# Kernel optimization log

Hardware: AMD Instinct MI355X
Metric: run time of the kernel (lower is better)

The kernel has to match this reference:

```python
import jax, jax.numpy as jnp
import numpy as np

B, S, IN, D, H, K, NLVL = 8, 1536, 32, 128, 4, 7, 2
DFF = 4 * D
DK = D // H
EPS = 1e-6


def setup_inputs() -> dict:
    key = jax.random.key(0)
    ks = jax.random.split(key, 24)
    rn = lambda k, sh, s=0.05: jax.random.normal(k, sh, jnp.float32) * s
    z = lambda sh: jnp.zeros(sh, jnp.float32)
    o = lambda sh: jnp.ones(sh, jnp.float32)
    return {
        'x': jax.random.normal(ks[0], (B, S, IN), jnp.float32),
        'enc_W': rn(ks[1], (IN, D)), 'enc_b': z((D,)),
        'ln_rnn_a': o((NLVL, D)), 'ln_rnn_b': z((NLVL, D)),
        'gru_Wih': rn(ks[2], (NLVL, 3 * D, D)), 'gru_Whh': rn(ks[3], (NLVL, 3 * D, D)),
        'gru_bih': z((NLVL, 3 * D)), 'gru_bhh': z((NLVL, 3 * D)),
        'ln_attn_a': o((NLVL, D)), 'ln_attn_b': z((NLVL, D)),
        'Wq': rn(ks[4], (NLVL, D, D)), 'bq': z((NLVL, D)),
        'Wk': rn(ks[5], (NLVL, D, D)), 'bk': z((NLVL, D)),
        'Wv': rn(ks[6], (NLVL, D, D)), 'bv': z((NLVL, D)),
        'Wo': rn(ks[7], (NLVL, D, D)), 'bo': z((NLVL, D)),
        'ln_ff_a': o((NLVL, D)), 'ln_ff_b': z((NLVL, D)),
        'ff_W1': rn(ks[8], (NLVL, D, DFF)), 'ff_b1': z((NLVL, DFF)),
        'ff_W2': rn(ks[9], (NLVL, DFF, D)), 'ff_b2': z((NLVL, D)),
        'out_W': rn(ks[10], (D, 1)), 'out_b': z((1,)),
    }


def layernorm(x, a, b):
    # faithful to torch code: unbiased std (ddof=1), divide by (std + eps)
    m = x.mean(-1, keepdims=True)
    s = jnp.std(x, axis=-1, ddof=1, keepdims=True)
    return a * (x - m) / (s + EPS) + b


def local_rnn(x, Wih, Whh, bih, bhh):
    # x: [B,S,D]. Window each position into its ksize-length causal window,
    # run a GRU over the window (scan over K steps, batched over B*S), keep last h.
    xp = jnp.pad(x, ((0, 0), (K - 1, 0), (0, 0)))            # zero left-pad
    win = jnp.stack([xp[:, i:i + S] for i in range(K)], 0)   # [K,B,S,D]

    def step(h, xt):
        gi = xt @ Wih.T + bih                                 # [B,S,3D]
        gh = h @ Whh.T + bhh
        ir, iz, inn = jnp.split(gi, 3, -1)
        hr, hz, hn = jnp.split(gh, 3, -1)
        r = jax.nn.sigmoid(ir + hr)
        zz = jax.nn.sigmoid(iz + hz)
        nn_ = jnp.tanh(inn + r * hn)
        return (1.0 - zz) * nn_ + zz * h, None

    h, _ = jax.lax.scan(step, jnp.zeros_like(x), win)
    return h


def mhpool(x, Wq, bq, Wk, bk, Wv, bv, Wo, bo):
    def heads(w, bb):
        return jnp.swapaxes((x @ w + bb).reshape(B, S, H, DK), 1, 2)  # [B,H,S,DK]
    q, k, v = heads(Wq, bq), heads(Wk, bk), heads(Wv, bv)
    scores = jnp.einsum('bhqd,bhkd->bhqk', q, k) / np.float32(np.sqrt(DK))
    mask = jnp.tril(jnp.ones((S, S), bool))
    scores = jnp.where(mask, scores, jnp.float32(-1e9))
    p = jax.nn.softmax(scores, axis=-1)
    o = jnp.einsum('bhqk,bhkd->bhqd', p, v)
    o = jnp.swapaxes(o, 1, 2).reshape(B, S, D)
    return o @ Wo + bo


def reference(x, enc_W, enc_b, ln_rnn_a, ln_rnn_b, gru_Wih, gru_Whh, gru_bih,
              gru_bhh, ln_attn_a, ln_attn_b, Wq, bq, Wk, bk, Wv, bv, Wo, bo,
              ln_ff_a, ln_ff_b, ff_W1, ff_b1, ff_W2, ff_b2, out_W, out_b):
    h = x @ enc_W + enc_b
    for i in range(NLVL):
        # LocalRNNLayer (pre-norm residual); LocalRNN.output Linear is unused in orig forward
        h = h + local_rnn(layernorm(h, ln_rnn_a[i], ln_rnn_b[i]),
                          gru_Wih[i], gru_Whh[i], gru_bih[i], gru_bhh[i])
        # MHPooling sublayer
        h = h + mhpool(layernorm(h, ln_attn_a[i], ln_attn_b[i]),
                       Wq[i], bq[i], Wk[i], bk[i], Wv[i], bv[i], Wo[i], bo[i])
        # PositionwiseFeedForward sublayer
        hn = layernorm(h, ln_ff_a[i], ln_ff_b[i])
        h = h + (jax.nn.relu(hn @ ff_W1[i] + ff_b1[i]) @ ff_W2[i] + ff_b2[i])
    return jax.nn.sigmoid(h @ out_W + out_b)
```

## Files before the change

### kernel.cpp

```cpp
#include <hip/hip_runtime.h>
#include <math.h>

#define DEV_INLINE __device__ __forceinline__

constexpr int B = 8, S = 1536, IN = 32, D = 128, NH = 4, KWIN = 7, NLVL = 2;
constexpr int DFF = 512, DKH = 32;
constexpr int M = B * S;
constexpr int MD = M * D;
constexpr float EPS = 1e-6f;

typedef unsigned short u16;
typedef __bf16 bf16x8 __attribute__((ext_vector_type(8)));
typedef float f32x4 __attribute__((ext_vector_type(4)));
typedef unsigned short u16x4 __attribute__((ext_vector_type(4)));

#define MFMA16(a, b, c) __builtin_amdgcn_mfma_f32_16x16x32_bf16(a, b, c, 0, 0, 0)

DEV_INLINE float sigmoidf_(float x) { return 1.f / (1.f + __expf(-x)); }

DEV_INLINE u16 f2bf(float f) {
    unsigned u = __builtin_bit_cast(unsigned, f);
    unsigned rnd = 0x7FFFu + ((u >> 16) & 1u);
    return (u16)((u + rnd) >> 16);
}
DEV_INLINE float b2f(u16 v) { return __builtin_bit_cast(float, (unsigned)v << 16); }

template <int KDIM>
DEV_INLINE void mfma_tile32(const u16* a0p, const u16* a1p, const u16* b0p, const u16* b1p,
                            f32x4& acc00, f32x4& acc01, f32x4& acc10, f32x4& acc11) {
    #pragma unroll
    for (int k0 = 0; k0 < KDIM; k0 += 32) {
        bf16x8 a0 = *(const bf16x8*)(a0p + k0);
        bf16x8 a1 = *(const bf16x8*)(a1p + k0);
        bf16x8 b0 = *(const bf16x8*)(b0p + k0);
        bf16x8 b1 = *(const bf16x8*)(b1p + k0);
        acc00 = MFMA16(a0, b0, acc00);
        acc01 = MFMA16(a0, b1, acc01);
        acc10 = MFMA16(a1, b0, acc10);
        acc11 = MFMA16(a1, b1, acc11);
    }
}

__global__ __launch_bounds__(256) void k_prep_enc(
    const float* __restrict__ Wih, const float* __restrict__ Whh,
    const float* __restrict__ Wq, const float* __restrict__ Wk,
    const float* __restrict__ Wv, const float* __restrict__ Wo,
    const float* __restrict__ W1, const float* __restrict__ W2,
    u16* __restrict__ Wih16, u16* __restrict__ Whh16,
    u16* __restrict__ Wqkv, u16* __restrict__ WoT,
    u16* __restrict__ W1T, u16* __restrict__ W2T,
    const float* __restrict__ x, const float* __restrict__ encW, const float* __restrict__ encb,
    const float* __restrict__ ga, const float* __restrict__ gb,
    float* __restrict__ h, u16* __restrict__ xnout) {
    __shared__ float xs[32][33];
    __shared__ float Ws[32][128];
    const int tid = threadIdx.x;
    if (blockIdx.x < 2304) {
        constexpr int SZ_GRU = NLVL * 384 * 128;
        constexpr int SZ_DD  = NLVL * 128 * 128;
        constexpr int SZ_FF  = NLVL * 128 * 512;
        int i = blockIdx.x * 256 + tid;
        if (i < SZ_GRU) { Wih16[i] = f2bf(Wih[i]); return; }
        i -= SZ_GRU;
        if (i < SZ_GRU) { Whh16[i] = f2bf(Whh[i]); return; }
        i -= SZ_GRU;
        if (i < 3 * SZ_DD) {
            int seg = i / SZ_DD, j = i - seg * SZ_DD;
            int lvl = j >> 14, rem = j & 16383, k = rem >> 7, n = rem & 127;
            const float* src = seg == 0 ? Wq : (seg == 1 ? Wk : Wv);
            Wqkv[(size_t)lvl * 384 * 128 + (size_t)(seg * 128 + n) * 128 + k] = f2bf(src[j]);
            return;
        }
        i -= 3 * SZ_DD;
        if (i < SZ_DD) {
            int lvl = i >> 14, rem = i & 16383, k = rem >> 7, n = rem & 127;
            WoT[(size_t)lvl * 16384 + n * 128 + k] = f2bf(Wo[i]); return;
        }
        i -= SZ_DD;
        if (i < SZ_FF) {
            int lvl = i >> 16, rem = i & 65535, k = rem >> 9, n = rem & 511;
            W1T[(size_t)lvl * 65536 + n * 128 + k] = f2bf(W1[i]); return;
        }
        i -= SZ_FF;
        if (i < SZ_FF) {
            int lvl = i >> 16, rem = i & 65535, k = rem >> 7, n = rem & 127;
            W2T[(size_t)lvl * 65536 + n * 512 + k] = f2bf(W2[i]); return;
        }
        return;
    }
    const int row0 = (blockIdx.x - 2304) * 32;
    for (int i = tid; i < 32 * 32; i += 256) xs[i >> 5][i & 31] = x[(size_t)row0 * IN + i];
    for (int i = tid; i < 32 * 128; i += 256) Ws[i >> 7][i & 127] = encW[i];
    __syncthreads();
    const int r = tid >> 3, cg = (tid & 7) * 16;
    float acc[16];
    #pragma unroll
    for (int j = 0; j < 16; ++j) acc[j] = encb[cg + j];
    for (int k = 0; k < IN; ++k) {
        const float xv = xs[r][k];
        #pragma unroll
        for (int j = 0; j < 16; ++j) acc[j] = fmaf(xv, Ws[k][cg + j], acc[j]);
    }
    float s = 0.f;
    #pragma unroll
    for (int j = 0; j < 16; ++j) s += acc[j];
    s += __shfl_xor(s, 1); s += __shfl_xor(s, 2); s += __shfl_xor(s, 4);
    const float mean = s * (1.f / D);
    float q = 0.f;
    #pragma unroll
    for (int j = 0; j < 16; ++j) { float d = acc[j] - mean; q += d * d; }
    q += __shfl_xor(q, 1); q += __shfl_xor(q, 2); q += __shfl_xor(q, 4);
    const float inv = 1.f / (sqrtf(q * (1.f / (D - 1))) + EPS);
    float* hp = h + (size_t)(row0 + r) * D + cg;
    u16* xp = xnout + (size_t)(row0 + r) * D + cg;
    #pragma unroll
    for (int jj = 0; jj < 4; ++jj) {
        float4 hv = make_float4(acc[4 * jj], acc[4 * jj + 1], acc[4 * jj + 2], acc[4 * jj + 3]);
        *(float4*)(hp + 4 * jj) = hv;
        u16x4 o;
        #pragma unroll
        for (int c = 0; c < 4; ++c)
            o[c] = f2bf(ga[cg + 4 * jj + c] * (acc[4 * jj + c] - mean) * inv + gb[cg + 4 * jj + c]);
        *(u16x4*)(xp + 4 * jj) = o;
    }
}

__global__ __launch_bounds__(512, 2) void k_gru_qkv(
    const u16* __restrict__ xn,
    const u16* __restrict__ Wih16,
    const u16* __restrict__ Whh16,
    const float* __restrict__ bih, const float* __restrict__ bhh,
    float* __restrict__ hout,
    const float* __restrict__ ga, const float* __restrict__ gb,
    const u16* __restrict__ Wqkv,
    const float* __restrict__ bq, const float* __restrict__ bk, const float* __restrict__ bv,
    u16* __restrict__ q16, u16* __restrict__ k16, u16* __restrict__ vt16) {
    constexpr int RB = 48;
    constexpr float QS = 0.17677669529663687f * 1.4426950408889634f;
    __shared__ __align__(16) u16 xnS[64 * 136];
    __shared__ __align__(16) u16 Gs[64 * 392];
    __shared__ __align__(16) u16 hs16[RB * 136];
    const int tid = threadIdx.x;
    const int wave = tid >> 6, lane = tid & 63;
    const int col16 = lane & 15, quad = lane >> 4;
    const int row0 = blockIdx.x * RB;
    const int ss0 = row0 % S;
    const int cc = wave * 16 + col16;

    for (int i = tid; i < 64 * 16; i += 512) {
        const int r = i >> 4, c8 = (i & 15) * 8;
        bf16x8 val = {};
        if (ss0 - 16 + r >= 0)
            val = *(const bf16x8*)(xn + (size_t)(row0 - 16 + r) * 128 + c8);
        *(bf16x8*)&xnS[r * 136 + c8] = val;
    }
    bf16x8 Breg[3][4];
    #pragma unroll
    for (int g = 0; g < 3; ++g)
        #pragma unroll
        for (int kc = 0; kc < 4; ++kc)
            Breg[g][kc] = *(const bf16x8*)(Whh16 + (size_t)(g * 128 + cc) * 128 + kc * 32 + quad * 8);
    float bi[3], bh[3];
    #pragma unroll
    for (int g = 0; g < 3; ++g) { bi[g] = bih[g * 128 + cc]; bh[g] = bhh[g * 128 + cc]; }
    __syncthreads();

    #pragma unroll
    for (int tt = wave; tt < 24; tt += 8) {
        const int rt = tt / 12, ct = tt - rt * 12;
        const u16* bp = Wih16 + (size_t)(ct * 32 + col16) * 128 + quad * 8;
        f32x4 a00 = {0.f, 0.f, 0.f, 0.f}, a01 = a00, a10 = a00, a11 = a00;
        #pragma unroll
        for (int k0 = 0; k0 < 128; k0 += 32) {
            bf16x8 af0 = *(const bf16x8*)&xnS[(rt * 32 + col16) * 136 + k0 + quad * 8];
            bf16x8 af1 = *(const bf16x8*)&xnS[(rt * 32 + 16 + col16) * 136 + k0 + quad * 8];
            bf16x8 b0 = *(const bf16x8*)(bp + k0);
            bf16x8 b1 = *(const bf16x8*)(bp + 16 * 128 + k0);
            a00 = MFMA16(af0, b0, a00);
            a01 = MFMA16(af0, b1, a01);
            a10 = MFMA16(af1, b0, a10);
            a11 = MFMA16(af1, b1, a11);
        }
        #pragma unroll
        for (int r = 0; r < 4; ++r) {
            const int gr0 = rt * 32 + quad * 4 + r, gr1 = gr0 + 16;
            Gs[gr0 * 392 + ct * 32 + col16]      = f2bf(a00[r]);
            Gs[gr0 * 392 + ct * 32 + 16 + col16] = f2bf(a01[r]);
            Gs[gr1 * 392 + ct * 32 + col16]      = f2bf(a10[r]);
            Gs[gr1 * 392 + ct * 32 + 16 + col16] = f2bf(a11[r]);
        }
    }
    float hp[12] = {};
    __syncthreads();

    for (int t = 0; t < KWIN; ++t) {
        const int shift = KWIN - 1 - t;
        f32x4 acc[3][3];
        #pragma unroll
        for (int rh = 0; rh < 3; ++rh)
            #pragma unroll
            for (int g = 0; g < 3; ++g) acc[rh][g] = {0.f, 0.f, 0.f, 0.f};
        if (t > 0) {
            bf16x8 af[3][4];
            #pragma unroll
            for (int rh = 0; rh < 3; ++rh)
                #pragma unroll
                for (int kc = 0; kc < 4; ++kc)
                    af[rh][kc] = *(const bf16x8*)&hs16[(rh * 16 + col16) * 136 + kc * 32 + quad * 8];
            __syncthreads();
            #pragma unroll
            for (int kc = 0; kc < 4; ++kc)
                #pragma unroll
                for (int g = 0; g < 3; ++g)
                    #pragma unroll
                    for (int rh = 0; rh < 3; ++rh)
                        acc[rh][g] = MFMA16(af[rh][kc], Breg[g][kc], acc[rh][g]);
        }
        const bool last = (t == KWIN - 1);
        #pragma unroll
        for (int rh = 0; rh < 3; ++rh) {
            #pragma unroll
            for (int r = 0; r < 4; ++r) {
                const int idx = rh * 4 + r;
                const int lrow = rh * 16 + quad * 4 + r;
                const int gr = lrow - shift + 16;
                const float xr  = b2f(Gs[gr * 392 + cc]);
                const float xz  = b2f(Gs[gr * 392 + 128 + cc]);
                const float xn_ = b2f(Gs[gr * 392 + 256 + cc]);
                const float rr = sigmoidf_(xr + bi[0] + acc[rh][0][r] + bh[0]);
                const float zz = sigmoidf_(xz + bi[1] + acc[rh][1][r] + bh[1]);
                const float e2 = __expf(2.f * (xn_ + bi[2] + rr * (acc[rh][2][r] + bh[2])));
                const float nn = 1.f - 2.f / (e2 + 1.f);
                const float hnew = (1.f - zz) * nn + zz * hp[idx];
                hp[idx] = hnew;
                if (!last) hs16[lrow * 136 + cc] = f2bf(hnew);
            }
        }
        __syncthreads();
    }
    float* hf = (float*)Gs;
    #pragma unroll
    for (int rh = 0; rh < 3; ++rh)
        #pragma unroll
        for (int r = 0; r < 4; ++r) {
            const int lrow = rh * 16 + quad * 4 + r;
            const float hv = hp[rh * 4 + r] + hout[(size_t)(row0 + lrow) * D + cc];
            hout[(size_t)(row0 + lrow) * D + cc] = hv;
            hf[lrow * 132 + cc] = hv;
        }
    __syncthreads();
    {
        const int r = tid >> 3;
        if (r < RB) {
            const int cg = (tid & 7) * 16;
            float vals[16];
            #pragma unroll
            for (int jj = 0; jj < 4; ++jj) {
                float4 v = *(const float4*)&hf[r * 132 + cg + 4 * jj];
                vals[4 * jj] = v.x; vals[4 * jj + 1] = v.y; vals[4 * jj + 2] = v.z; vals[4 * jj + 3] = v.w;
            }
            float s = 0.f;
            #pragma unroll
            for (int j = 0; j < 16; ++j) s += vals[j];
            s += __shfl_xor(s, 1); s += __shfl_xor(s, 2); s += __shfl_xor(s, 4);
            const float mean = s * (1.f / D);
            float q = 0.f;
            #pragma unroll
            for (int j = 0; j < 16; ++j) { float d = vals[j] - mean; q += d * d; }
            q += __shfl_xor(q, 1); q += __shfl_xor(q, 2); q += __shfl_xor(q, 4);
            const float inv = 1.f / (sqrtf(q * (1.f / (D - 1))) + EPS);
            #pragma unroll
            for (int jj = 0; jj < 4; ++jj) {
                u16x4 o;
                #pragma unroll
                for (int c = 0; c < 4; ++c)
                    o[c] = f2bf(ga[cg + 4 * jj + c] * (vals[4 * jj + c] - mean) * inv + gb[cg + 4 * jj + c]);
                *(u16x4*)&hs16[r * 136 + cg + 4 * jj] = o;
            }
        }
    }
    __syncthreads();
    for (int tt = wave; tt < 36; tt += 8) {
        const int rt = tt / 12, ct = tt - rt * 12;
        const int seg = ct >> 2;
        const int c0 = (ct & 3) * 32;
        const u16* bp = Wqkv + (size_t)(seg * 128 + c0 + col16) * 128 + quad * 8;
        f32x4 a0 = {0.f, 0.f, 0.f, 0.f}, a1 = a0;
        #pragma unroll
        for (int k0 = 0; k0 < 128; k0 += 32) {
            bf16x8 af = *(const bf16x8*)&hs16[(rt * 16 + col16) * 136 + k0 + quad * 8];
            bf16x8 b0 = *(const bf16x8*)(bp + k0);
            bf16x8 b1 = *(const bf16x8*)(bp + 16 * 128 + k0);
            a0 = MFMA16(af, b0, a0);
            a1 = MFMA16(af, b1, a1);
        }
        if (seg < 2) {
            const float* bias = seg == 0 ? bq : bk;
            const float sc = seg == 0 ? QS : 1.f;
            const float bv0 = bias[c0 + col16], bv1 = bias[c0 + 16 + col16];
            u16* o16 = seg == 0 ? q16 : k16;
            #pragma unroll
            for (int r = 0; r < 4; ++r) {
                const size_t gr = (size_t)(row0 + rt * 16 + quad * 4 + r) * 128;
                o16[gr + c0 + col16]      = f2bf((a0[r] + bv0) * sc);
                o16[gr + c0 + 16 + col16] = f2bf((a1[r] + bv1) * sc);
            }
        } else {
            const float bv0 = bv[c0 + col16], bv1 = bv[c0 + 16 + col16];
            const int bb = row0 / S, ssv = row0 - bb * S + rt * 16;
            const int ca = c0 + col16, cb = c0 + 16 + col16;
            u16* pa = vt16 + ((size_t)((bb * NH + (ca >> 5)) * 32 + (ca & 31))) * S + ssv;
            u16* pb = vt16 + ((size_t)((bb * NH + (cb >> 5)) * 32 + (cb & 31))) * S + ssv;
            #pragma unroll
            for (int r = 0; r < 4; ++r) {
                pa[quad * 4 + r] = f2bf(a0[r] + bv0);
                pb[quad * 4 + r] = f2bf(a1[r] + bv1);
            }
        }
    }
}

__global__ __launch_bounds__(256) void k_attn_mfma(
    const u16* Qb, const u16* __restrict__ Kb,
    const u16* __restrict__ Vt, u16* O16) {
    const int wave = threadIdx.x >> 6, lane = threadIdx.x & 63;
    const int p = blockIdx.x;
    const int bh = blockIdx.y;
    const int b = bh >> 2, hh = bh & 3;
    const int col = lane & 15, quad = lane >> 4;

    __shared__ __align__(16) u16 Pb[4][32][40];
    __shared__ float Om[4][32][33];
    __shared__ float Lm[4][32];
    u16 (* __restrict__ P)[40] = Pb[wave];

    const u16* Kbase = Kb + (size_t)b * S * 128 + hh * 32;
    const u16* Vbase = Vt + (size_t)bh * 32 * S;

    #pragma unroll
    for (int half = 0; half < 2; ++half) {
        const int qt = half == 0 ? p : 47 - p;
        const int q0 = qt * 32;
        const int nkt = qt + 1;
        const u16* qp = Qb + (size_t)(b * S + q0 + col) * 128 + hh * 32 + quad * 8;
        const bf16x8 qf0 = *(const bf16x8*)qp;
        const bf16x8 qf1 = *(const bf16x8*)(qp + 16 * 128);
        f32x4 o00 = {0.f, 0.f, 0.f, 0.f}, o01 = o00, o10 = o00, o11 = o00;
        float lsum[8] = {};
        int kt = wave;
        bf16x8 kf0 = {}, kf1 = {}, vf0 = {}, vf1 = {};
        if (kt < nkt) {
            const u16* kp = Kbase + (size_t)(kt * 32 + col) * 128 + quad * 8;
            kf0 = *(const bf16x8*)kp;
            kf1 = *(const bf16x8*)(kp + 16 * 128);
            const u16* vp = Vbase + (size_t)col * S + kt * 32 + quad * 8;
            vf0 = *(const bf16x8*)vp;
            vf1 = *(const bf16x8*)(vp + 16 * S);
        }
        while (kt < nkt) {
            const int ktn = kt + 4;
            bf16x8 nk0 = kf0, nk1 = kf1, nv0 = vf0, nv1 = vf1;
            if (ktn < nkt) {
                const u16* kp = Kbase + (size_t)(ktn * 32 + col) * 128 + quad * 8;
                nk0 = *(const bf16x8*)kp;
                nk1 = *(const bf16x8*)(kp + 16 * 128);
                const u16* vp = Vbase + (size_t)col * S + ktn * 32 + quad * 8;
                nv0 = *(const bf16x8*)vp;
                nv1 = *(const bf16x8*)(vp + 16 * S);
            }
            f32x4 z = {0.f, 0.f, 0.f, 0.f};
            f32x4 s00 = MFMA16(qf0, kf0, z);
            f32x4 s01 = MFMA16(qf0, kf1, z);
            f32x4 s10 = MFMA16(qf1, kf0, z);
            f32x4 s11 = MFMA16(qf1, kf1, z);
            const bool diag = (kt == qt);
            const int k0g = kt * 32;
            #pragma unroll
            for (int r = 0; r < 4; ++r) {
                const int lr = quad * 4 + r;
                float p00 = __builtin_amdgcn_exp2f(s00[r]);
                float p01 = __builtin_amdgcn_exp2f(s01[r]);
                float p10 = __builtin_amdgcn_exp2f(s10[r]);
                float p11 = __builtin_amdgcn_exp2f(s11[r]);
                if (diag) {
                    const int qg0 = q0 + lr, qg1 = q0 + 16 + lr;
                    if (k0g + col > qg0)      p00 = 0.f;
                    if (k0g + 16 + col > qg0) p01 = 0.f;
                    if (k0g + col > qg1)      p10 = 0.f;
                    if (k0g + 16 + col > qg1) p11 = 0.f;
                }
                lsum[r]     += p00 + p01;
                lsum[4 + r] += p10 + p11;
                P[lr][col]           = f2bf(p00);
                P[lr][16 + col]      = f2bf(p01);
                P[16 + lr][col]      = f2bf(p10);
                P[16 + lr][16 + col] = f2bf(p11);
            }
            const bf16x8 pa0 = *(const bf16x8*)&P[col][quad * 8];
            const bf16x8 pa1 = *(const bf16x8*)&P[16 + col][quad * 8];
            o00 = MFMA16(pa0, vf0, o00);
            o01 = MFMA16(pa0, vf1, o01);
            o10 = MFMA16(pa1, vf0, o10);
            o11 = MFMA16(pa1, vf1, o11);
            kf0 = nk0; kf1 = nk1; vf0 = nv0; vf1 = nv1;
            kt = ktn;
        }
        #pragma unroll
        for (int i = 0; i < 8; ++i) {
            float v = lsum[i];
            v += __shfl_xor(v, 1); v += __shfl_xor(v, 2);
            v += __shfl_xor(v, 4); v += __shfl_xor(v, 8);
            lsum[i] = v;
        }
        #pragma unroll
        for (int r = 0; r < 4; ++r) {
            const int lr = quad * 4 + r;
            Om[wave][lr][col]           = o00[r];
            Om[wave][lr][16 + col]      = o01[r];
            Om[wave][16 + lr][col]      = o10[r];
            Om[wave][16 + lr][16 + col] = o11[r];
        }
        if (col == 0) {
            #pragma unroll
            for (int i = 0; i < 8; ++i)
                Lm[wave][(i >> 2) * 16 + quad * 4 + (i & 3)] = lsum[i];
        }
        __syncthreads();
        {
            const int tr = threadIdx.x >> 3, tc = (threadIdx.x & 7) * 4;
            const float inv = 1.f / (Lm[0][tr] + Lm[1][tr] + Lm[2][tr] + Lm[3][tr]);
            u16x4 outv;
            #pragma unroll
            for (int c = 0; c < 4; ++c) {
                const float o = Om[0][tr][tc + c] + Om[1][tr][tc + c] +
                                Om[2][tr][tc + c] + Om[3][tr][tc + c];
                outv[c] = f2bf(o * inv);
            }
            *(u16x4*)(O16 + (size_t)(b * S + q0 + tr) * 128 + hh * 32 + tc) = outv;
        }
        __syncthreads();
    }
}

template <bool LAST>
__global__ __launch_bounds__(256) void k_mho_ffn(
    const u16* __restrict__ ao, const u16* __restrict__ WoT, const float* __restrict__ bo,
    float* __restrict__ hio,
    const float* __restrict__ ga1, const float* __restrict__ gb1,
    const u16* __restrict__ W1T, const float* __restrict__ b1,
    const u16* __restrict__ W2T, const float* __restrict__ b2,
    const float* __restrict__ ga2, const float* __restrict__ gb2, u16* __restrict__ xnout,
    const float* __restrict__ outW, const float* __restrict__ outb, float* __restrict__ outp) {
    __shared__ float hL[32 * 132];
    __shared__ __align__(16) u16 xnL[32 * 136];
    __shared__ __align__(16) u16 Ls[32 * 520];
    const int tid = threadIdx.x;
    const int wave = tid >> 6, lane = tid & 63;
    const int col16 = lane & 15, quad = lane >> 4;
    const int row0 = blockIdx.x * 32;
    const int c0 = wave * 32;

    {
        const u16* a0p = ao + (size_t)(row0 + col16) * 128 + quad * 8;
        const u16* b0p = WoT + (size_t)(c0 + col16) * 128 + quad * 8;
        f32x4 acc00 = {0.f, 0.f, 0.f, 0.f}, acc01 = acc00, acc10 = acc00, acc11 = acc00;
        mfma_tile32<128>(a0p, a0p + 16 * 128, b0p, b0p + 16 * 128, acc00, acc01, acc10, acc11);
        const float bv0 = bo[c0 + col16];
        const float bv1 = bo[c0 + 16 + col16];
        #pragma unroll
        for (int r = 0; r < 4; ++r) {
            const int l0 = quad * 4 + r, l1 = 16 + quad * 4 + r;
            const size_t g0 = (size_t)(row0 + l0) * D, g1 = (size_t)(row0 + l1) * D;
            hL[l0 * 132 + c0 + col16]      = acc00[r] + bv0 + hio[g0 + c0 + col16];
            hL[l0 * 132 + c0 + 16 + col16] = acc01[r] + bv1 + hio[g0 + c0 + 16 + col16];
            hL[l1 * 132 + c0 + col16]      = acc10[r] + bv0 + hio[g1 + c0 + col16];
            hL[l1 * 132 + c0 + 16 + col16] = acc11[r] + bv1 + hio[g1 + c0 + 16 + col16];
        }
    }
    __syncthreads();
    {
        const int r = tid >> 3, cg = (tid & 7) * 16;
        float vals[16];
        #pragma unroll
        for (int jj = 0; jj < 4; ++jj) {
            float4 v = *(const float4*)&hL[r * 132 + cg + 4 * jj];
            vals[4 * jj] = v.x; vals[4 * jj + 1] = v.y; vals[4 * jj + 2] = v.z; vals[4 * jj + 3] = v.w;
        }
        float s = 0.f;
        #pragma unroll
        for (int j = 0; j < 16; ++j) s += vals[j];
        s += __shfl_xor(s, 1); s += __shfl_xor(s, 2); s += __shfl_xor(s, 4);
        const float mean = s * (1.f / D);
        float q = 0.f;
        #pragma unroll
        for (int j = 0; j < 16; ++j) { float d = vals[j] - mean; q += d * d; }
        q += __shfl_xor(q, 1); q += __shfl_xor(q, 2); q += __shfl_xor(q, 4);
        const float inv = 1.f / (sqrtf(q * (1.f / (D - 1))) + EPS);
        #pragma unroll
        for (int jj = 0; jj < 4; ++jj) {
            u16x4 o;
            #pragma unroll
            for (int c = 0; c < 4; ++c)
                o[c] = f2bf(ga1[cg + 4 * jj + c] * (vals[4 * jj + c] - mean) * inv + gb1[cg + 4 * jj + c]);
            *(u16x4*)&xnL[r * 136 + cg + 4 * jj] = o;
        }
    }
    __syncthreads();
    #pragma unroll
    for (int ct = 0; ct < 4; ++ct) {
        const int c0f = wave * 128 + ct * 32;
        const u16* b0p = W1T + (size_t)(c0f + col16) * 128 + quad * 8;
        f32x4 acc00 = {0.f, 0.f, 0.f, 0.f}, acc01 = acc00, acc10 = acc00, acc11 = acc00;
        #pragma unroll
        for (int k0 = 0; k0 < 128; k0 += 32) {
            bf16x8 a0 = *(const bf16x8*)&xnL[col16 * 136 + k0 + quad * 8];
            bf16x8 a1 = *(const bf16x8*)&xnL[(16 + col16) * 136 + k0 + quad * 8];
            bf16x8 b0 = *(const bf16x8*)(b0p + k0);
            bf16x8 b1 = *(const bf16x8*)(b0p + 16 * 128 + k0);
            acc00 = MFMA16(a0, b0, acc00);
            acc01 = MFMA16(a0, b1, acc01);
            acc10 = MFMA16(a1, b0, acc10);
            acc11 = MFMA16(a1, b1, acc11);
        }
        const float bv0 = b1[c0f + col16];
        const float bv1 = b1[c0f + 16 + col16];
        #pragma unroll
        for (int r = 0; r < 4; ++r) {
            const int l0 = quad * 4 + r, l1 = 16 + quad * 4 + r;
            Ls[l0 * 520 + c0f + col16]      = f2bf(fmaxf(acc00[r] + bv0, 0.f));
            Ls[l0 * 520 + c0f + 16 + col16] = f2bf(fmaxf(acc01[r] + bv1, 0.f));
            Ls[l1 * 520 + c0f + col16]      = f2bf(fmaxf(acc10[r] + bv0, 0.f));
            Ls[l1 * 520 + c0f + 16 + col16] = f2bf(fmaxf(acc11[r] + bv1, 0.f));
        }
    }
    __syncthreads();
    {
        f32x4 acc00 = {0.f, 0.f, 0.f, 0.f}, acc01 = acc00, acc10 = acc00, acc11 = acc00;
        #pragma unroll
        for (int k0 = 0; k0 < 512; k0 += 32) {
            bf16x8 a0 = *(const bf16x8*)&Ls[col16 * 520 + k0 + quad * 8];
            bf16x8 a1 = *(const bf16x8*)&Ls[(16 + col16) * 520 + k0 + quad * 8];
            const u16* bp = W2T + (size_t)(c0 + col16) * 512 + k0 + quad * 8;
            bf16x8 b0 = *(const bf16x8*)bp;
            bf16x8 b1v = *(const bf16x8*)(bp + 16 * 512);
            acc00 = MFMA16(a0, b0, acc00);
            acc01 = MFMA16(a0, b1v, acc01);
            acc10 = MFMA16(a1, b0, acc10);
            acc11 = MFMA16(a1, b1v, acc11);
        }
        const float bv0 = b2[c0 + col16];
        const float bv1 = b2[c0 + 16 + col16];
        #pragma unroll
        for (int r = 0; r < 4; ++r) {
            const int l0 = quad * 4 + r, l1 = 16 + quad * 4 + r;
            const size_t g0 = (size_t)(row0 + l0) * D, g1 = (size_t)(row0 + l1) * D;
            const float v00 = acc00[r] + bv0 + hL[l0 * 132 + c0 + col16];
            const float v01 = acc01[r] + bv1 + hL[l0 * 132 + c0 + 16 + col16];
            const float v10 = acc10[r] + bv0 + hL[l1 * 132 + c0 + col16];
            const float v11 = acc11[r] + bv1 + hL[l1 * 132 + c0 + 16 + col16];
            hio[g0 + c0 + col16]      = v00;
            hio[g0 + c0 + 16 + col16] = v01;
            hio[g1 + c0 + col16]      = v10;
            hio[g1 + c0 + 16 + col16] = v11;
            hL[l0 * 132 + c0 + col16]      = v00;
            hL[l0 * 132 + c0 + 16 + col16] = v01;
            hL[l1 * 132 + c0 + col16]      = v10;
            hL[l1 * 132 + c0 + 16 + col16] = v11;
        }
    }
    __syncthreads();
    {
        const int r = tid >> 3, cg = (tid & 7) * 16;
        float vals[16];
        #pragma unroll
        for (int jj = 0; jj < 4; ++jj) {
            float4 v = *(const float4*)&hL[r * 132 + cg + 4 * jj];
            vals[4 * jj] = v.x; vals[4 * jj + 1] = v.y; vals[4 * jj + 2] = v.z; vals[4 * jj + 3] = v.w;
        }
        if constexpr (LAST) {
            float dot = 0.f;
            #pragma unroll
            for (int j = 0; j < 16; ++j) dot += vals[j] * outW[cg + j];
            dot += __shfl_xor(dot, 1); dot += __shfl_xor(dot, 2); dot += __shfl_xor(dot, 4);
            if ((tid & 7) == 0) outp[row0 + r] = sigmoidf_(dot + outb[0]);
        } else {
            float s = 0.f;
            #pragma unroll
            for (int j = 0; j < 16; ++j) s += vals[j];
            s += __shfl_xor(s, 1); s += __shfl_xor(s, 2); s += __shfl_xor(s, 4);
            const float mean = s * (1.f / D);
            float q = 0.f;
            #pragma unroll
            for (int j = 0; j < 16; ++j) { float d = vals[j] - mean; q += d * d; }
            q += __shfl_xor(q, 1); q += __shfl_xor(q, 2); q += __shfl_xor(q, 4);
            const float inv = 1.f / (sqrtf(q * (1.f / (D - 1))) + EPS);
            u16* xp = xnout + (size_t)(row0 + r) * D + cg;
            #pragma unroll
            for (int jj = 0; jj < 4; ++jj) {
                u16x4 o;
                #pragma unroll
                for (int c = 0; c < 4; ++c)
                    o[c] = f2bf(ga2[cg + 4 * jj + c] * (vals[4 * jj + c] - mean) * inv + gb2[cg + 4 * jj + c]);
                *(u16x4*)(xp + 4 * jj) = o;
            }
        }
    }
}

extern "C" void kernel_launch(void* const* d_in, const int* in_sizes, int n_in,
                              void* d_out, int out_size, void* d_ws, size_t ws_size,
                              hipStream_t stream) {
    const float* x       = (const float*)d_in[0];
    const float* enc_W   = (const float*)d_in[1];
    const float* enc_b   = (const float*)d_in[2];
    const float* ln_rnn_a = (const float*)d_in[3];
    const float* ln_rnn_b = (const float*)d_in[4];
    const float* gru_Wih = (const float*)d_in[5];
    const float* gru_Whh = (const float*)d_in[6];
    const float* gru_bih = (const float*)d_in[7];
    const float* gru_bhh = (const float*)d_in[8];
    const float* ln_attn_a = (const float*)d_in[9];
    const float* ln_attn_b = (const float*)d_in[10];
    const float* Wq = (const float*)d_in[11];
    const float* bq = (const float*)d_in[12];
    const float* Wk = (const float*)d_in[13];
    const float* bk = (const float*)d_in[14];
    const float* Wv = (const float*)d_in[15];
    const float* bv = (const float*)d_in[16];
    const float* Wo = (const float*)d_in[17];
    const float* bo = (const float*)d_in[18];
    const float* ln_ff_a = (const float*)d_in[19];
    const float* ln_ff_b = (const float*)d_in[20];
    const float* ff_W1 = (const float*)d_in[21];
    const float* ff_b1 = (const float*)d_in[22];
    const float* ff_W2 = (const float*)d_in[23];
    const float* ff_b2 = (const float*)d_in[24];
    const float* out_W = (const float*)d_in[25];
    const float* out_b = (const float*)d_in[26];

    float* h   = (float*)d_ws;
    u16* pool  = (u16*)(h + MD);
    u16* xn16  = pool + (size_t)3 * MD;
    u16* Wih16 = xn16 + MD;
    u16* Whh16 = Wih16 + NLVL * 384 * D;
    u16* Wqkv  = Whh16 + NLVL * 384 * D;
    u16* WoT   = Wqkv + NLVL * 384 * D;
    u16* W1T   = WoT + NLVL * D * D;
    u16* W2T   = W1T + NLVL * D * DFF;

    u16* q16   = pool;
    u16* k16   = pool + MD;
    u16* vt16  = pool + (size_t)2 * MD;
    u16* ao16  = q16;

    k_prep_enc<<<2688, 256, 0, stream>>>(
        gru_Wih, gru_Whh, Wq, Wk, Wv, Wo, ff_W1, ff_W2,
        Wih16, Whh16, Wqkv, WoT, W1T, W2T,
        x, enc_W, enc_b, ln_rnn_a, ln_rnn_b, h, xn16);

    for (int lvl = 0; lvl < NLVL; ++lvl) {
        k_gru_qkv<<<256, 512, 0, stream>>>(
            xn16, Wih16 + lvl * 384 * D, Whh16 + lvl * 384 * D,
            gru_bih + lvl * 384, gru_bhh + lvl * 384,
            h, ln_attn_a + lvl * D, ln_attn_b + lvl * D,
            Wqkv + lvl * 384 * D, bq + lvl * D, bk + lvl * D, bv + lvl * D,
            q16, k16, vt16);

        k_attn_mfma<<<dim3(24, 32), 256, 0, stream>>>(q16, k16, vt16, ao16);

        if (lvl + 1 < NLVL) {
            k_mho_ffn<false><<<M / 32, 256, 0, stream>>>(
                ao16, WoT + lvl * D * D, bo + lvl * D, h,
                ln_ff_a + lvl * D, ln_ff_b + lvl * D,
                W1T + lvl * D * DFF, ff_b1 + lvl * DFF,
                W2T + lvl * DFF * D, ff_b2 + lvl * D,
                ln_rnn_a + (lvl + 1) * D, ln_rnn_b + (lvl + 1) * D, xn16,
                nullptr, nullptr, nullptr);
        } else {
            k_mho_ffn<true><<<M / 32, 256, 0, stream>>>(
                ao16, WoT + lvl * D * D, bo + lvl * D, h,
                ln_ff_a + lvl * D, ln_ff_b + lvl * D,
                W1T + lvl * D * DFF, ff_b1 + lvl * DFF,
                W2T + lvl * DFF * D, ff_b2 + lvl * D,
                nullptr, nullptr, nullptr,
                out_W, out_b, (float*)d_out);
        }
    }
}
```

Baseline: 320.0 us.

## Double-buffer GRU hidden state, interleave gate layout, use fast rcp/exp2 intrinsics

```diff
diff --git a/kernel.cpp b/kernel.cpp
--- a/kernel.cpp
+++ b/kernel.cpp
@@ -8,6 +8,7 @@
 constexpr int M = B * S;
 constexpr int MD = M * D;
 constexpr float EPS = 1e-6f;
+constexpr float LOG2E = 1.4426950408889634f;
 
 typedef unsigned short u16;
 typedef __bf16 bf16x8 __attribute__((ext_vector_type(8)));
@@ -16,7 +17,11 @@
 
 #define MFMA16(a, b, c) __builtin_amdgcn_mfma_f32_16x16x32_bf16(a, b, c, 0, 0, 0)
 
+DEV_INLINE float frcp(float x) { return __builtin_amdgcn_rcpf(x); }
+DEV_INLINE float fexp2(float x) { return __builtin_amdgcn_exp2f(x); }
 DEV_INLINE float sigmoidf_(float x) { return 1.f / (1.f + __expf(-x)); }
+DEV_INLINE float fsigmoid(float x) { return frcp(1.f + fexp2(-LOG2E * x)); }
+DEV_INLINE float ftanh(float x) { return 1.f - 2.f * frcp(fexp2(2.f * LOG2E * x) + 1.f); }
 
 DEV_INLINE u16 f2bf(float f) {
     unsigned u = __builtin_bit_cast(unsigned, f);
@@ -136,10 +141,12 @@
     const float* __restrict__ bq, const float* __restrict__ bk, const float* __restrict__ bv,
     u16* __restrict__ q16, u16* __restrict__ k16, u16* __restrict__ vt16) {
     constexpr int RB = 48;
+    constexpr int GST = 516;
     constexpr float QS = 0.17677669529663687f * 1.4426950408889634f;
     __shared__ __align__(16) u16 xnS[64 * 136];
-    __shared__ __align__(16) u16 Gs[64 * 392];
-    __shared__ __align__(16) u16 hs16[RB * 136];
+    __shared__ __align__(16) u16 Gs[64 * GST];
+    __shared__ __align__(16) u16 hsA[RB * 136];
+    __shared__ __align__(16) u16 hsB[RB * 136];
     const int tid = threadIdx.x;
     const int wave = tid >> 6, lane = tid & 63;
     const int col16 = lane & 15, quad = lane >> 4;
@@ -168,6 +175,8 @@
     #pragma unroll
     for (int tt = wave; tt < 24; tt += 8) {
         const int rt = tt / 12, ct = tt - rt * 12;
+        const int gg = ct >> 2;
+        const int cb = (ct & 3) * 32;
         const u16* bp = Wih16 + (size_t)(ct * 32 + col16) * 128 + quad * 8;
         f32x4 a00 = {0.f, 0.f, 0.f, 0.f}, a01 = a00, a10 = a00, a11 = a00;
         #pragma unroll
@@ -184,10 +193,10 @@
         #pragma unroll
         for (int r = 0; r < 4; ++r) {
             const int gr0 = rt * 32 + quad * 4 + r, gr1 = gr0 + 16;
-            Gs[gr0 * 392 + ct * 32 + col16]      = f2bf(a00[r]);
-            Gs[gr0 * 392 + ct * 32 + 16 + col16] = f2bf(a01[r]);
-            Gs[gr1 * 392 + ct * 32 + col16]      = f2bf(a10[r]);
-            Gs[gr1 * 392 + ct * 32 + 16 + col16] = f2bf(a11[r]);
+            Gs[gr0 * GST + (cb + col16) * 4 + gg]      = f2bf(a00[r]);
+            Gs[gr0 * GST + (cb + 16 + col16) * 4 + gg] = f2bf(a01[r]);
+            Gs[gr1 * GST + (cb + col16) * 4 + gg]      = f2bf(a10[r]);
+            Gs[gr1 * GST + (cb + 16 + col16) * 4 + gg] = f2bf(a11[r]);
         }
     }
     float hp[12] = {};
@@ -195,6 +204,16 @@
 
     for (int t = 0; t < KWIN; ++t) {
         const int shift = KWIN - 1 - t;
+        u16* wbuf = (t & 1) ? hsB : hsA;
+        const u16* rbuf = (t & 1) ? hsA : hsB;
+        u16x4 gv[12];
+        #pragma unroll
+        for (int rh = 0; rh < 3; ++rh)
+            #pragma unroll
+            for (int r = 0; r < 4; ++r) {
+                const int lrow = rh * 16 + quad * 4 + r;
+                gv[rh * 4 + r] = *(const u16x4*)&Gs[(lrow - shift + 16) * GST + cc * 4];
+            }
         f32x4 acc[3][3];
         #pragma unroll
         for (int rh = 0; rh < 3; ++rh)
@@ -206,8 +225,7 @@
             for (int rh = 0; rh < 3; ++rh)
                 #pragma unroll
                 for (int kc = 0; kc < 4; ++kc)
-                    af[rh][kc] = *(const bf16x8*)&hs16[(rh * 16 + col16) * 136 + kc * 32 + quad * 8];
-            __syncthreads();
+                    af[rh][kc] = *(const bf16x8*)&rbuf[(rh * 16 + col16) * 136 + kc * 32 + quad * 8];
             #pragma unroll
             for (int kc = 0; kc < 4; ++kc)
                 #pragma unroll
@@ -223,17 +241,15 @@
             for (int r = 0; r < 4; ++r) {
                 const int idx = rh * 4 + r;
                 const int lrow = rh * 16 + quad * 4 + r;
-                const int gr = lrow - shift + 16;
-                const float xr  = b2f(Gs[gr * 392 + cc]);
-                const float xz  = b2f(Gs[gr * 392 + 128 + cc]);
-                const float xn_ = b2f(Gs[gr * 392 + 256 + cc]);
-                const float rr = sigmoidf_(xr + bi[0] + acc[rh][0][r] + bh[0]);
-                const float zz = sigmoidf_(xz + bi[1] + acc[rh][1][r] + bh[1]);
-                const float e2 = __expf(2.f * (xn_ + bi[2] + rr * (acc[rh][2][r] + bh[2])));
-                const float nn = 1.f - 2.f / (e2 + 1.f);
+                const float xr  = b2f(gv[idx][0]);
+                const float xz  = b2f(gv[idx][1]);
+                const float xn_ = b2f(gv[idx][2]);
+                const float rr = fsigmoid(xr + bi[0] + acc[rh][0][r] + bh[0]);
+                const float zz = fsigmoid(xz + bi[1] + acc[rh][1][r] + bh[1]);
+                const float nn = ftanh(xn_ + bi[2] + rr * (acc[rh][2][r] + bh[2]));
                 const float hnew = (1.f - zz) * nn + zz * hp[idx];
                 hp[idx] = hnew;
-                if (!last) hs16[lrow * 136 + cc] = f2bf(hnew);
+                if (!last) wbuf[lrow * 136 + cc] = f2bf(hnew);
             }
         }
         __syncthreads();
@@ -268,14 +284,14 @@
             #pragma unroll
             for (int j = 0; j < 16; ++j) { float d = vals[j] - mean; q += d * d; }
             q += __shfl_xor(q, 1); q += __shfl_xor(q, 2); q += __shfl_xor(q, 4);
-            const float inv = 1.f / (sqrtf(q * (1.f / (D - 1))) + EPS);
+            const float inv = frcp(sqrtf(q * (1.f / (D - 1))) + EPS);
             #pragma unroll
             for (int jj = 0; jj < 4; ++jj) {
                 u16x4 o;
                 #pragma unroll
                 for (int c = 0; c < 4; ++c)
                     o[c] = f2bf(ga[cg + 4 * jj + c] * (vals[4 * jj + c] - mean) * inv + gb[cg + 4 * jj + c]);
-                *(u16x4*)&hs16[r * 136 + cg + 4 * jj] = o;
+                *(u16x4*)&hsA[r * 136 + cg + 4 * jj] = o;
             }
         }
     }
@@ -288,7 +304,7 @@
         f32x4 a0 = {0.f, 0.f, 0.f, 0.f}, a1 = a0;
         #pragma unroll
         for (int k0 = 0; k0 < 128; k0 += 32) {
-            bf16x8 af = *(const bf16x8*)&hs16[(rt * 16 + col16) * 136 + k0 + quad * 8];
+            bf16x8 af = *(const bf16x8*)&hsA[(rt * 16 + col16) * 136 + k0 + quad * 8];
             bf16x8 b0 = *(const bf16x8*)(bp + k0);
             bf16x8 b1 = *(const bf16x8*)(bp + 16 * 128 + k0);
             a0 = MFMA16(af, b0, a0);
@@ -378,10 +394,10 @@
             #pragma unroll
             for (int r = 0; r < 4; ++r) {
                 const int lr = quad * 4 + r;
-                float p00 = __builtin_amdgcn_exp2f(s00[r]);
-                float p01 = __builtin_amdgcn_exp2f(s01[r]);
-                float p10 = __builtin_amdgcn_exp2f(s10[r]);
-                float p11 = __builtin_amdgcn_exp2f(s11[r]);
+                float p00 = fexp2(s00[r]);
+                float p01 = fexp2(s01[r]);
+                float p10 = fexp2(s10[r]);
+                float p11 = fexp2(s11[r]);
                 if (diag) {
                     const int qg0 = q0 + lr, qg1 = q0 + 16 + lr;
                     if (k0g + col > qg0)      p00 = 0.f;
@@ -428,7 +444,7 @@
         __syncthreads();
         {
             const int tr = threadIdx.x >> 3, tc = (threadIdx.x & 7) * 4;
-            const float inv = 1.f / (Lm[0][tr] + Lm[1][tr] + Lm[2][tr] + Lm[3][tr]);
+            const float inv = frcp(Lm[0][tr] + Lm[1][tr] + Lm[2][tr] + Lm[3][tr]);
             u16x4 outv;
             #pragma unroll
             for (int c = 0; c < 4; ++c) {
@@ -495,7 +511,7 @@
         #pragma unroll
         for (int j = 0; j < 16; ++j) { float d = vals[j] - mean; q += d * d; }
         q += __shfl_xor(q, 1); q += __shfl_xor(q, 2); q += __shfl_xor(q, 4);
-        const float inv = 1.f / (sqrtf(q * (1.f / (D - 1))) + EPS);
+        const float inv = frcp(sqrtf(q * (1.f / (D - 1))) + EPS);
         #pragma unroll
         for (int jj = 0; jj < 4; ++jj) {
             u16x4 o;
@@ -593,7 +609,7 @@
             #pragma unroll
             for (int j = 0; j < 16; ++j) { float d = vals[j] - mean; q += d * d; }
             q += __shfl_xor(q, 1); q += __shfl_xor(q, 2); q += __shfl_xor(q, 4);
-            const float inv = 1.f / (sqrtf(q * (1.f / (D - 1))) + EPS);
+            const float inv = frcp(sqrtf(q * (1.f / (D - 1))) + EPS);
             u16* xp = xnout + (size_t)(row0 + r) * D + cg;
             #pragma unroll
             for (int jj = 0; jj < 4; ++jj) {
@@ -659,7 +675,7 @@
         x, enc_W, enc_b, ln_rnn_a, ln_rnn_b, h, xn16);
 
     for (int lvl = 0; lvl < NLVL; ++lvl) {
-        k_gru_qkv<<<256, 512, 0, stream>>>(
+        k_gru_qkv<<<M / 48, 512, 0, stream>>>(
             xn16, Wih16 + lvl * 384 * D, Whh16 + lvl * 384 * D,
             gru_bih + lvl * 384, gru_bhh + lvl * 384,
             h, ln_attn_a + lvl * D, ln_attn_b + lvl * D,
```

After: 293.0 us. 8.4% less time.
